# Optimization experiments

Measured on AMD Instinct MI355X. Metric: run time of the kernel, lower is better.

The kernel has to match this reference:

```python
import jax, jax.numpy as jnp
import numpy as np


def _sobel_filters():
    # fil is the 3x3 smoothing kernel [[1,2,1],[2,4,2],[1,2,1]]
    fil = np.array([[1, 2, 1], [2, 4, 2], [1, 2, 1]], dtype=np.float32)
    fx = np.zeros((3, 3, 3), dtype=np.float32)
    fx[0, :, :] = fil
    fx[2, :, :] = -fil
    fy = np.zeros((3, 3, 3), dtype=np.float32)
    fy[:, 0, :] = fil
    fy[:, 2, :] = -fil
    fz = np.zeros((3, 3, 3), dtype=np.float32)
    fz[:, :, 0] = fil
    fz[:, :, 2] = -fil
    # Stack the three fixed (non-learned) filters as 3 output channels: [O=3, I=1, 3,3,3]
    return jnp.asarray(np.stack([fx, fy, fz])[:, None])


_FILT = _sobel_filters()
_DN = ('NCDHW', 'OIDHW', 'NCDHW')


def _grad3d(v):
    # v: [N,1,D,H,W] -> [N,3,D,H,W], padding=1 == SAME for 3x3x3 stride 1
    return jax.lax.conv_general_dilated(
        v, _FILT.astype(v.dtype), window_strides=(1, 1, 1),
        padding='SAME', dimension_numbers=_DN)


def setup_inputs() -> dict:
    key = jax.random.key(0)
    k1, k2 = jax.random.split(key)
    shape = (2, 1, 160, 192, 224)
    x = jax.random.normal(k1, shape, dtype=jnp.float32)
    y = jax.random.normal(k2, shape, dtype=jnp.float32)
    return {"x": x, "y": y}


def reference(x, y):
    gx = _grad3d(x)  # [N,3,D,H,W]
    gy = _grad3d(y)
    d2 = (gx - gy) ** 2
    # sum over the 3 directions of the per-direction MSE
    return jnp.sum(jnp.mean(d2, axis=(0, 2, 3, 4)))
```

## Files before the change

kernel.cpp:

```cpp
#include <hip/hip_runtime.h>
#include <stdint.h>


#define N_  2
#define D_  160
#define H_  192
#define W_  224
#define PS  (H_ * W_)

#define TD  10
#define TH  8
constexpr float SCALE = 1.0f / ((float)N_ * D_ * H_ * W_);

__device__ __forceinline__ float4 f4add(float4 a, float4 b) {
    return make_float4(a.x + b.x, a.y + b.y, a.z + b.z, a.w + b.w);
}
__device__ __forceinline__ float4 f4sub(float4 a, float4 b) {
    return make_float4(a.x - b.x, a.y - b.y, a.z - b.z, a.w - b.w);
}
__device__ __forceinline__ float4 f4fma(float k, float4 a, float4 b) {
    return make_float4(fmaf(k, a.x, b.x), fmaf(k, a.y, b.y),
                       fmaf(k, a.z, b.z), fmaf(k, a.w, b.w));
}

__global__ __launch_bounds__(256, 3)
void grad_loss_kernel(const float* __restrict__ x, const float* __restrict__ y,
                      float* __restrict__ out) {
    __shared__ float wsum[4];

    const int tid  = threadIdx.x;
    const int lane = tid & 63;
    const int wv   = tid >> 6;

    const int nchunks = D_ / TD;
    const int nb = blockIdx.z / nchunks;
    const int d0 = (blockIdx.z % nchunks) * TD;
    const int h0w = blockIdx.y * TH + 2 * wv;

    const float* vbx = x + (size_t)nb * ((size_t)D_ * PS);
    const float* vby = y + (size_t)nb * ((size_t)D_ * PS);

    const bool wact = lane < 56;
    const int lo4c = (lane < 56 ? lane : 55) * 4;
    int off[4];
    float rmask[4];
    #pragma unroll
    for (int r = 0; r < 4; ++r) {
        int gh  = h0w - 1 + r;
        int ghc = min(max(gh, 0), H_ - 1);
        off[r]   = ghc * W_ + lo4c;
        rmask[r] = (((unsigned)gh < (unsigned)H_) && wact) ? 1.f : 0.f;
    }

    float4 XR[8];
    auto loadp = [&](int p) {
        int pc = min(max(p, 0), D_ - 1);
        const float* bx = vbx + (size_t)pc * PS;
        const float* by = vby + (size_t)pc * PS;
        #pragma unroll
        for (int r = 0; r < 4; ++r) {
            XR[2 * r]     = *(const float4*)(bx + off[r]);
            XR[2 * r + 1] = *(const float4*)(by + off[r]);
        }
    };

    float4 A0[2], A1[2], A2[2], B0[2], B1[2], B2[2];
    const float4 z4 = make_float4(0.f, 0.f, 0.f, 0.f);
    #pragma unroll
    for (int j = 0; j < 2; ++j) { A0[j]=A1[j]=A2[j]=B0[j]=B1[j]=B2[j]=z4; }
    float acc = 0.f;

    loadp(d0 - 1);

    for (int it = 0; it < TD + 2; ++it) {
        const int q = d0 - 1 + it;
        const float pm = (q >= 0 && q < D_) ? 1.f : 0.f;

        float4 v[4];
        #pragma unroll
        for (int r = 0; r < 4; ++r) {
            const float m = rmask[r] * pm;
            v[r] = make_float4((XR[2*r].x - XR[2*r+1].x) * m,
                               (XR[2*r].y - XR[2*r+1].y) * m,
                               (XR[2*r].z - XR[2*r+1].z) * m,
                               (XR[2*r].w - XR[2*r+1].w) * m);
        }

        if (it <= TD) loadp(d0 + it);

        float4 n0[2], n1[2], n2[2];
        #pragma unroll
        for (int r = 0; r < 4; ++r) {
            const float4 vv = v[r];
            float Lm = __shfl_up(vv.w, 1, 64);
            float Rp = __shfl_down(vv.x, 1, 64);
            if (lane == 0) Lm = 0.f;
            const float4 s = make_float4(Lm + 2.f * vv.x + vv.y,
                                         vv.x + 2.f * vv.y + vv.z,
                                         vv.y + 2.f * vv.z + vv.w,
                                         vv.z + 2.f * vv.w + Rp);
            const float4 g = make_float4(Lm - vv.y, vv.x - vv.z,
                                         vv.y - vv.w, vv.z - Rp);
            if (r == 0) { n0[0] = s;                 n1[0] = s;
                          n2[0] = g; }
            if (r == 1) { n0[0] = f4fma(2.f, s, n0[0]);
                          n2[0] = f4fma(2.f, g, n2[0]);
                          n0[1] = s;                 n1[1] = s;
                          n2[1] = g; }
            if (r == 2) { n0[0] = f4add(n0[0], s);   n1[0] = f4sub(n1[0], s);
                          n2[0] = f4add(n2[0], g);
                          n0[1] = f4fma(2.f, s, n0[1]);
                          n2[1] = f4fma(2.f, g, n2[1]); }
            if (r == 3) { n0[1] = f4add(n0[1], s);   n1[1] = f4sub(n1[1], s);
                          n2[1] = f4add(n2[1], g); }
        }

        if (it >= 2) {
            #pragma unroll
            for (int j = 0; j < 2; ++j) {
                const float4 gx = f4sub(A0[j], n0[j]);
                const float4 gy = f4add(f4fma(2.f, B1[j], A1[j]), n1[j]);
                const float4 gz = f4add(f4fma(2.f, B2[j], A2[j]), n2[j]);
                acc = fmaf(gx.x, gx.x, acc); acc = fmaf(gx.y, gx.y, acc);
                acc = fmaf(gx.z, gx.z, acc); acc = fmaf(gx.w, gx.w, acc);
                acc = fmaf(gy.x, gy.x, acc); acc = fmaf(gy.y, gy.y, acc);
                acc = fmaf(gy.z, gy.z, acc); acc = fmaf(gy.w, gy.w, acc);
                acc = fmaf(gz.x, gz.x, acc); acc = fmaf(gz.y, gz.y, acc);
                acc = fmaf(gz.z, gz.z, acc); acc = fmaf(gz.w, gz.w, acc);
            }
        }

        #pragma unroll
        for (int j = 0; j < 2; ++j) {
            A0[j] = B0[j]; A1[j] = B1[j]; A2[j] = B2[j];
            B0[j] = n0[j]; B1[j] = n1[j]; B2[j] = n2[j];
        }
    }

    #pragma unroll
    for (int off_ = 32; off_ > 0; off_ >>= 1)
        acc += __shfl_xor(acc, off_, 64);
    if (lane == 0) wsum[wv] = acc;
    __syncthreads();
    if (tid == 0) {
        float s = (wsum[0] + wsum[1]) + (wsum[2] + wsum[3]);
        atomicAdd(out, s * SCALE);
    }
}

extern "C" void kernel_launch(void* const* d_in, const int* in_sizes, int n_in,
                              void* d_out, int out_size, void* d_ws, size_t ws_size,
                              hipStream_t stream) {
    const float* x = (const float*)d_in[0];
    const float* y = (const float*)d_in[1];
    float* out = (float*)d_out;

    hipMemsetAsync(out, 0, sizeof(float), stream);

    dim3 block(256);
    dim3 grid(1,
              H_ / TH,
              N_ * (D_ / TD));
    grad_loss_kernel<<<grid, block, 0, stream>>>(x, y, out);
}
```

Baseline: 134.3 us.

## Compute four output rows per wave to cut halo reloads

Each wave now produces four H rows instead of two, loading six input rows per plane instead of four, and the block drops from four waves to two. The halo read overhead per output row falls from 2x to 1.5x. The next plane's loads now issue after the current plane's smoothing pass, and lanes 56-63 skip the accumulation. In exchange, register pressure rises (12 float4 loads plus 24 float4 history values), launch bounds change to 128 threads with 2 blocks per SM, and there are fewer waves in flight.

```diff
diff --git a/kernel.cpp b/kernel.cpp
--- a/kernel.cpp
+++ b/kernel.cpp
@@ -9,6 +9,7 @@
 #define PS  (H_ * W_)
 
 #define TD  10
+#define RW  4
 #define TH  8
 constexpr float SCALE = 1.0f / ((float)N_ * D_ * H_ * W_);
 
@@ -23,10 +24,10 @@
                        fmaf(k, a.z, b.z), fmaf(k, a.w, b.w));
 }
 
-__global__ __launch_bounds__(256, 3)
+__global__ __launch_bounds__(128, 2)
 void grad_loss_kernel(const float* __restrict__ x, const float* __restrict__ y,
                       float* __restrict__ out) {
-    __shared__ float wsum[4];
+    __shared__ float wsum[2];
 
     const int tid  = threadIdx.x;
     const int lane = tid & 63;
@@ -35,39 +36,39 @@
     const int nchunks = D_ / TD;
     const int nb = blockIdx.z / nchunks;
     const int d0 = (blockIdx.z % nchunks) * TD;
-    const int h0w = blockIdx.y * TH + 2 * wv;
+    const int h0w = blockIdx.y * TH + RW * wv;
 
     const float* vbx = x + (size_t)nb * ((size_t)D_ * PS);
     const float* vby = y + (size_t)nb * ((size_t)D_ * PS);
 
     const bool wact = lane < 56;
     const int lo4c = (lane < 56 ? lane : 55) * 4;
-    int off[4];
-    float rmask[4];
+    int off[6];
+    float rmask[6];
     #pragma unroll
-    for (int r = 0; r < 4; ++r) {
+    for (int r = 0; r < 6; ++r) {
         int gh  = h0w - 1 + r;
         int ghc = min(max(gh, 0), H_ - 1);
         off[r]   = ghc * W_ + lo4c;
         rmask[r] = (((unsigned)gh < (unsigned)H_) && wact) ? 1.f : 0.f;
     }
 
-    float4 XR[8];
+    float4 XR[12];
     auto loadp = [&](int p) {
         int pc = min(max(p, 0), D_ - 1);
         const float* bx = vbx + (size_t)pc * PS;
         const float* by = vby + (size_t)pc * PS;
         #pragma unroll
-        for (int r = 0; r < 4; ++r) {
+        for (int r = 0; r < 6; ++r) {
             XR[2 * r]     = *(const float4*)(bx + off[r]);
             XR[2 * r + 1] = *(const float4*)(by + off[r]);
         }
     };
 
-    float4 A0[2], A1[2], A2[2], B0[2], B1[2], B2[2];
+    float4 A0[RW], A1[RW], A2[RW], B0[RW], B1[RW], B2[RW];
     const float4 z4 = make_float4(0.f, 0.f, 0.f, 0.f);
     #pragma unroll
-    for (int j = 0; j < 2; ++j) { A0[j]=A1[j]=A2[j]=B0[j]=B1[j]=B2[j]=z4; }
+    for (int j = 0; j < RW; ++j) { A0[j]=A1[j]=A2[j]=B0[j]=B1[j]=B2[j]=z4; }
     float acc = 0.f;
 
     loadp(d0 - 1);
@@ -76,22 +77,14 @@
         const int q = d0 - 1 + it;
         const float pm = (q >= 0 && q < D_) ? 1.f : 0.f;
 
-        float4 v[4];
+        float4 n0[RW], n1[RW], n2[RW];
         #pragma unroll
-        for (int r = 0; r < 4; ++r) {
+        for (int r = 0; r < 6; ++r) {
             const float m = rmask[r] * pm;
-            v[r] = make_float4((XR[2*r].x - XR[2*r+1].x) * m,
-                               (XR[2*r].y - XR[2*r+1].y) * m,
-                               (XR[2*r].z - XR[2*r+1].z) * m,
-                               (XR[2*r].w - XR[2*r+1].w) * m);
-        }
-
-        if (it <= TD) loadp(d0 + it);
-
-        float4 n0[2], n1[2], n2[2];
-        #pragma unroll
-        for (int r = 0; r < 4; ++r) {
-            const float4 vv = v[r];
+            const float4 vv = make_float4((XR[2*r].x - XR[2*r+1].x) * m,
+                                          (XR[2*r].y - XR[2*r+1].y) * m,
+                                          (XR[2*r].z - XR[2*r+1].z) * m,
+                                          (XR[2*r].w - XR[2*r+1].w) * m);
             float Lm = __shfl_up(vv.w, 1, 64);
             float Rp = __shfl_down(vv.x, 1, 64);
             if (lane == 0) Lm = 0.f;
@@ -101,23 +94,26 @@
                                          vv.z + 2.f * vv.w + Rp);
             const float4 g = make_float4(Lm - vv.y, vv.x - vv.z,
                                          vv.y - vv.w, vv.z - Rp);
-            if (r == 0) { n0[0] = s;                 n1[0] = s;
-                          n2[0] = g; }
-            if (r == 1) { n0[0] = f4fma(2.f, s, n0[0]);
-                          n2[0] = f4fma(2.f, g, n2[0]);
-                          n0[1] = s;                 n1[1] = s;
-                          n2[1] = g; }
-            if (r == 2) { n0[0] = f4add(n0[0], s);   n1[0] = f4sub(n1[0], s);
-                          n2[0] = f4add(n2[0], g);
-                          n0[1] = f4fma(2.f, s, n0[1]);
-                          n2[1] = f4fma(2.f, g, n2[1]); }
-            if (r == 3) { n0[1] = f4add(n0[1], s);   n1[1] = f4sub(n1[1], s);
-                          n2[1] = f4add(n2[1], g); }
+            #pragma unroll
+            for (int j = 0; j < RW; ++j) {
+                if (r == j) {
+                    n0[j] = s; n1[j] = s; n2[j] = g;
+                } else if (r == j + 1) {
+                    n0[j] = f4fma(2.f, s, n0[j]);
+                    n2[j] = f4fma(2.f, g, n2[j]);
+                } else if (r == j + 2) {
+                    n0[j] = f4add(n0[j], s);
+                    n1[j] = f4sub(n1[j], s);
+                    n2[j] = f4add(n2[j], g);
+                }
+            }
         }
 
-        if (it >= 2) {
+        if (it <= TD) loadp(d0 + it);
+
+        if (it >= 2 && wact) {
             #pragma unroll
-            for (int j = 0; j < 2; ++j) {
+            for (int j = 0; j < RW; ++j) {
                 const float4 gx = f4sub(A0[j], n0[j]);
                 const float4 gy = f4add(f4fma(2.f, B1[j], A1[j]), n1[j]);
                 const float4 gz = f4add(f4fma(2.f, B2[j], A2[j]), n2[j]);
@@ -131,7 +127,7 @@
         }
 
         #pragma unroll
-        for (int j = 0; j < 2; ++j) {
+        for (int j = 0; j < RW; ++j) {
             A0[j] = B0[j]; A1[j] = B1[j]; A2[j] = B2[j];
             B0[j] = n0[j]; B1[j] = n1[j]; B2[j] = n2[j];
         }
@@ -143,8 +139,7 @@
     if (lane == 0) wsum[wv] = acc;
     __syncthreads();
     if (tid == 0) {
-        float s = (wsum[0] + wsum[1]) + (wsum[2] + wsum[3]);
-        atomicAdd(out, s * SCALE);
+        atomicAdd(out, (wsum[0] + wsum[1]) * SCALE);
     }
 }
 
@@ -157,7 +152,7 @@
 
     hipMemsetAsync(out, 0, sizeof(float), stream);
 
-    dim3 block(256);
+    dim3 block(128);
     dim3 grid(1,
               H_ / TH,
               N_ * (D_ / TD));
```

Result: no change. 133.7 us (-0.5%).
